# Optimization experiments

Hardware: AMD Instinct MI355X
Metric: run time of the kernel (lower is better)

Reference implementation:

```python
import jax, jax.numpy as jnp
import numpy as np

H = 16
D_MODEL = 1024
D_K = D_MODEL // H
B, S = 4, 2048


def setup_inputs() -> dict:
    key = jax.random.key(0)
    ks = jax.random.split(key, 8)
    scale = 1.0 / np.sqrt(D_MODEL)
    return {
        "query": jax.random.normal(ks[0], (B, S, D_MODEL), dtype=jnp.float32),
        "key": jax.random.normal(ks[1], (B, S, D_MODEL), dtype=jnp.float32),
        "value": jax.random.normal(ks[2], (B, S, D_MODEL), dtype=jnp.float32),
        "A": jnp.zeros((1,), dtype=jnp.float32),
        "Wq": jax.random.normal(ks[3], (D_MODEL, D_MODEL), dtype=jnp.float32) * scale,
        "bq": jnp.zeros((D_MODEL,), dtype=jnp.float32),
        "Wk": jax.random.normal(ks[4], (D_MODEL, D_MODEL), dtype=jnp.float32) * scale,
        "bk": jnp.zeros((D_MODEL,), dtype=jnp.float32),
        "Wv": jax.random.normal(ks[5], (D_MODEL, D_MODEL), dtype=jnp.float32) * scale,
        "bv": jnp.zeros((D_MODEL,), dtype=jnp.float32),
        "Wo": jax.random.normal(ks[6], (D_MODEL, D_MODEL), dtype=jnp.float32) * scale,
        "bo": jnp.zeros((D_MODEL,), dtype=jnp.float32),
    }


def reference(query, key, value, A, Wq, bq, Wk, bk, Wv, bv, Wo, bo):
    nb = query.shape[0]

    def proj(x, W, b):
        # torch Linear: x @ W.T + b, then view(B, S, H, D_K) and transpose -> [B, H, S, D_K]
        y = jnp.einsum('bsd,ed->bse', x, W) + b
        return y.reshape(nb, -1, H, D_K).transpose(0, 2, 1, 3)

    q = proj(query, Wq, bq)
    k = proj(key, Wk, bk)
    v = proj(value, Wv, bv)

    # NOTE: original code has NO 1/sqrt(d_k) scaling, no mask, no dropout.
    scores = jnp.einsum('bhqd,bhkd->bhqk', q, k)  # [B,H,S,S]
    p_attn = jax.nn.softmax(scores, axis=-1)
    x = jnp.einsum('bhqk,bhkd->bhqd', p_attn, v)  # [B,H,S,D_K]

    x = x.transpose(0, 2, 1, 3).reshape(nb, -1, H * D_K)  # [B,S,d_model]
    out = jnp.einsum('bsd,ed->bse', x, Wo) + bo
    loss = jnp.asarray(0.0, dtype=out.dtype)
    return (out, loss)
```

## Files before the change

### kernel.cpp

```cpp
#include <hip/hip_runtime.h>

typedef unsigned short u16;
typedef _Float16 half8 __attribute__((ext_vector_type(8)));
typedef _Float16 h2 __attribute__((ext_vector_type(2)));
typedef float f32x4 __attribute__((ext_vector_type(4)));
typedef u16 u16x4 __attribute__((ext_vector_type(4)));
typedef u16 u16x8 __attribute__((ext_vector_type(8)));

#define MFMAH(a, b, c) __builtin_amdgcn_mfma_f32_16x16x32_f16(a, b, c, 0, 0, 0)

constexpr float LOG2E = 1.44269504088896f;
constexpr float THR = 12.0f;

__device__ __forceinline__ u16 f2h(float f) {
  _Float16 h = (_Float16)f;
  return __builtin_bit_cast(u16, h);
}
__device__ __forceinline__ h2 pkrtz(float a, float b) {
  return __builtin_bit_cast(h2, __builtin_amdgcn_cvt_pkrtz(a, b));
}
__device__ __forceinline__ void gload_lds16(const void* g, void* l) {
  __builtin_amdgcn_global_load_lds(
      (const __attribute__((address_space(1))) void*)g,
      (__attribute__((address_space(3))) void*)l,
      16, 0, 0);
}

__device__ __forceinline__ int swz(int row, int q) { return row * 32 + ((q ^ ((row >> 1) & 3)) << 3); }

__device__ __forceinline__ void conv_block(const float* __restrict__ in,
                                           u16* __restrict__ out, int i) {
  const float4 a = reinterpret_cast<const float4*>(in)[2 * i];
  const float4 b = reinterpret_cast<const float4*>(in)[2 * i + 1];
  u16x8 o;
  o[0] = f2h(a.x); o[1] = f2h(a.y); o[2] = f2h(a.z); o[3] = f2h(a.w);
  o[4] = f2h(b.x); o[5] = f2h(b.y); o[6] = f2h(b.z); o[7] = f2h(b.w);
  reinterpret_cast<u16x8*>(out)[i] = o;
}

__global__ __launch_bounds__(256) void conv_w4(const float* __restrict__ w0,
                                               const float* __restrict__ w1,
                                               const float* __restrict__ w2,
                                               const float* __restrict__ w3,
                                               u16* __restrict__ o0, u16* __restrict__ o1,
                                               u16* __restrict__ o2, u16* __restrict__ o3,
                                               int n8) {
  int i = blockIdx.x * 256 + threadIdx.x;
  const int stride = gridDim.x * 256;
  for (; i < 4 * n8; i += stride) {
    const int sel = i / n8, j = i - sel * n8;
    if (sel == 0) conv_block(w0, o0, j);
    else if (sel == 1) conv_block(w1, o1, j);
    else if (sel == 2) conv_block(w2, o2, j);
    else conv_block(w3, o3, j);
  }
}

__global__ __launch_bounds__(256) void proj_gemm(
    const float* __restrict__ Aq, const float* __restrict__ Ak, const float* __restrict__ Avv,
    const u16* __restrict__ Wq, const u16* __restrict__ Wk, const u16* __restrict__ Wv,
    const float* __restrict__ bq, const float* __restrict__ bk, const float* __restrict__ bv,
    u16* __restrict__ Cq, u16* __restrict__ Ck, u16* __restrict__ Cvv) {
  __shared__ u16 As[2][4096];
  __shared__ u16 Bs[2][4096];
  const int tid = threadIdx.x;
  const int lane = tid & 63, l16 = lane & 15, lhi = lane >> 4;
  const int wid = tid >> 6, wm = wid >> 1, wn = wid & 1;
  const int id = blockIdx.x + (blockIdx.y << 3) + (blockIdx.z << 9);
  const int xcd = id & 7;
  const int slot = id >> 3;
  const int by = ((slot & 7) << 3) | xcd;
  const int rest = slot >> 3;
  const int bx = rest & 7;
  const int z = rest >> 3;
  const int bm0 = by * 128, bn0 = bx * 128;

  const float* Af = (z == 0) ? Aq : ((z == 1) ? Ak : Avv);
  const u16* Bw = (z == 0) ? Wq : ((z == 1) ? Wk : Wv);
  const float* bias = (z == 0) ? bq : ((z == 1) ? bk : bv);
  u16* C = (z == 0) ? Cq : ((z == 1) ? Ck : Cvv);
  const float scale = (z == 0) ? LOG2E : 1.0f;

  const int c0 = tid, c1 = tid + 256;
  const u16* Bg0 = Bw + (size_t)(bn0 + (c0 >> 2)) * 1024 + (((c0 & 3) ^ ((c0 >> 3) & 3)) << 3);
  const u16* Bg1 = Bw + (size_t)(bn0 + (c1 >> 2)) * 1024 + (((c1 & 3) ^ ((c1 >> 3) & 3)) << 3);
  const int arow = tid >> 2, aq = tid & 3;
  const float* Ar = Af + (size_t)(bm0 + arow) * 1024 + aq * 8;
  const int awoff = swz(arow, aq);

  f32x4 acc[4][4] = {};
  float4 an[4];

#define LOADA(kt)                                                          \
  do {                                                                     \
    an[0] = *reinterpret_cast<const float4*>(Ar + (kt));                   \
    an[1] = *reinterpret_cast<const float4*>(Ar + (kt) + 4);               \
    an[2] = *reinterpret_cast<const float4*>(Ar + (kt) + 64 * 1024);       \
    an[3] = *reinterpret_cast<const float4*>(Ar + (kt) + 64 * 1024 + 4);   \
  } while (0)
#define STAGEB(buf, kt)                                                    \
  do {                                                                     \
    gload_lds16(Bg0 + (kt), &Bs[buf][c0 * 8]);                             \
    gload_lds16(Bg1 + (kt), &Bs[buf][c1 * 8]);                             \
  } while (0)
#define WRITEA(buf)                                                        \
  do {                                                                     \
    union { u16x8 u; h2 h[4]; } w0_, w1_;                                  \
    w0_.h[0] = pkrtz(an[0].x, an[0].y); w0_.h[1] = pkrtz(an[0].z, an[0].w);\
    w0_.h[2] = pkrtz(an[1].x, an[1].y); w0_.h[3] = pkrtz(an[1].z, an[1].w);\
    w1_.h[0] = pkrtz(an[2].x, an[2].y); w1_.h[1] = pkrtz(an[2].z, an[2].w);\
    w1_.h[2] = pkrtz(an[3].x, an[3].y); w1_.h[3] = pkrtz(an[3].z, an[3].w);\
    u16* dst_ = &As[buf][awoff];                                           \
    *reinterpret_cast<u16x8*>(dst_) = w0_.u;                               \
    *reinterpret_cast<u16x8*>(dst_ + 64 * 32) = w1_.u;                     \
  } while (0)

  LOADA(0);
  STAGEB(0, 0);
  WRITEA(0);
  __syncthreads();

  for (int ki = 0; ki < 32; ++ki) {
    const int cur = ki & 1, nxt = cur ^ 1;
    if (ki < 31) {
      LOADA((ki + 1) * 32);
      STAGEB(nxt, (ki + 1) * 32);
    }
    half8 af[4], bf[4];
#pragma unroll
    for (int f = 0; f < 4; ++f)
      af[f] = *reinterpret_cast<const half8*>(&As[cur][swz(wm * 64 + f * 16 + l16, lhi)]);
#pragma unroll
    for (int f = 0; f < 4; ++f)
      bf[f] = *reinterpret_cast<const half8*>(&Bs[cur][swz(wn * 64 + f * 16 + l16, lhi)]);
#pragma unroll
    for (int i = 0; i < 4; ++i)
#pragma unroll
      for (int j = 0; j < 4; ++j)
        acc[i][j] = MFMAH(af[i], bf[j], acc[i][j]);
    if (ki < 31) WRITEA(nxt);
    __syncthreads();
  }
#undef LOADA
#undef STAGEB
#undef WRITEA

#pragma unroll
  for (int i = 0; i < 4; ++i) {
    const int m0 = bm0 + wm * 64 + i * 16 + lhi * 4;
#pragma unroll
    for (int j = 0; j < 4; ++j) {
      const int n = bn0 + wn * 64 + j * 16 + l16;
      const float bb = bias[n];
      if (z == 2) {
        u16x4 pack;
#pragma unroll
        for (int r = 0; r < 4; ++r) pack[r] = f2h(acc[i][j][r] + bb);
        const int head = (m0 >> 11) * 16 + (n >> 6);
        const int s0 = m0 & 2047;
        const int d = n & 63;
        const int within =
            ((s0 >> 5) & 1) * 2048 + d * 32 + ((s0 >> 2) & 3) * 8 + ((s0 >> 4) & 1) * 4;
        const int sw = within ^ ((d & 7) << 3);
        const size_t idx = (size_t)head * 131072 + (size_t)(s0 >> 6) * 4096 + sw;
        *reinterpret_cast<u16x4*>(&C[idx]) = pack;
      } else {
#pragma unroll
        for (int r = 0; r < 4; ++r) {
          const int m = m0 + r;
          const size_t idx =
              ((size_t)((m >> 11) * 16 + (n >> 6)) * 2048 + (m & 2047)) * 64 + (n & 63);
          C[idx] = f2h((acc[i][j][r] + bb) * scale);
        }
      }
    }
  }
}

__global__ __launch_bounds__(256) void out_gemm(const u16* __restrict__ A,
                                                const u16* __restrict__ Bw,
                                                const float* __restrict__ bias,
                                                float* __restrict__ C) {
  __shared__ u16 As[2][4096];
  __shared__ u16 Bs[2][4096];
  const int tid = threadIdx.x;
  const int lane = tid & 63, l16 = lane & 15, lhi = lane >> 4;
  const int wid = tid >> 6, wm = wid >> 1, wn = wid & 1;
  const int id = blockIdx.x + (blockIdx.y << 3);
  const int xcd = id & 7, slot = id >> 3;
  const int by = ((slot & 7) << 3) | xcd;
  const int bx = slot >> 3;
  const int bm0 = by * 128, bn0 = bx * 128;

  const int c0 = tid, c1 = tid + 256;
  const u16* Ag0 = A + (size_t)(bm0 + (c0 >> 2)) * 1024 + (((c0 & 3) ^ ((c0 >> 3) & 3)) << 3);
  const u16* Ag1 = A + (size_t)(bm0 + (c1 >> 2)) * 1024 + (((c1 & 3) ^ ((c1 >> 3) & 3)) << 3);
  const u16* Bg0 = Bw + (size_t)(bn0 + (c0 >> 2)) * 1024 + (((c0 & 3) ^ ((c0 >> 3) & 3)) << 3);
  const u16* Bg1 = Bw + (size_t)(bn0 + (c1 >> 2)) * 1024 + (((c1 & 3) ^ ((c1 >> 3) & 3)) << 3);

  f32x4 acc[4][4] = {};

#define STAGE16(buf, kt)                                  \
  do {                                                    \
    gload_lds16(Ag0 + (kt), &As[buf][c0 * 8]);            \
    gload_lds16(Ag1 + (kt), &As[buf][c1 * 8]);            \
    gload_lds16(Bg0 + (kt), &Bs[buf][c0 * 8]);            \
    gload_lds16(Bg1 + (kt), &Bs[buf][c1 * 8]);            \
  } while (0)

  STAGE16(0, 0);
  __syncthreads();
  for (int ki = 0; ki < 32; ++ki) {
    const int cur = ki & 1;
    if (ki < 31) STAGE16(cur ^ 1, (ki + 1) * 32);
    half8 af[4], bf[4];
#pragma unroll
    for (int f = 0; f < 4; ++f)
      af[f] = *reinterpret_cast<const half8*>(&As[cur][swz(wm * 64 + f * 16 + l16, lhi)]);
#pragma unroll
    for (int f = 0; f < 4; ++f)
      bf[f] = *reinterpret_cast<const half8*>(&Bs[cur][swz(wn * 64 + f * 16 + l16, lhi)]);
#pragma unroll
    for (int i = 0; i < 4; ++i)
#pragma unroll
      for (int j = 0; j < 4; ++j)
        acc[i][j] = MFMAH(af[i], bf[j], acc[i][j]);
    __syncthreads();
  }
#undef STAGE16

#pragma unroll
  for (int i = 0; i < 4; ++i) {
    const int m0 = bm0 + wm * 64 + i * 16 + lhi * 4;
#pragma unroll
    for (int j = 0; j < 4; ++j) {
      const int n = bn0 + wn * 64 + j * 16 + l16;
      const float bb = bias[n];
#pragma unroll
      for (int r = 0; r < 4; ++r)
        C[(size_t)(m0 + r) * 1024 + n] = acc[i][j][r] + bb;
    }
  }
  if (id == 0 && tid == 0) C[(size_t)8192 * 1024] = 0.0f;
}

__global__ __launch_bounds__(256, 4) void attn_fwd(const u16* __restrict__ Q,
                                                   const u16* __restrict__ Kh,
                                                   const u16* __restrict__ VL,
                                                   u16* __restrict__ X) {
  __shared__ u16 Ks[2][4096];
  __shared__ u16 Vs[2][4096];

  const int tid = threadIdx.x, lane = tid & 63, w = tid >> 6;
  const int l16 = lane & 15, lhi = lane >> 4;
  const int blk = blockIdx.x;
  const int xcd = blk & 7, wi = blk >> 3;
  const int bh = (xcd << 3) | (wi >> 4);
  const int qt = wi & 15;
  const int b = bh >> 4, h = bh & 15;

  const size_t qrow0 = (size_t)bh * 2048 + qt * 128 + w * 32;
  half8 qf[2][2];
#pragma unroll
  for (int fq = 0; fq < 2; ++fq)
#pragma unroll
    for (int ks = 0; ks < 2; ++ks)
      qf[fq][ks] = *reinterpret_cast<const half8*>(
          &Q[(qrow0 + fq * 16 + l16) * 64 + ks * 32 + lhi * 8]);

  f32x4 o[2][4] = {};
  float mrow[2] = {-1e30f, -1e30f};
  float ssum[2] = {0.0f, 0.0f};

  const u16* Kb = Kh + (size_t)bh * 2048 * 64;
  const u16* VLh = VL + (size_t)bh * 64 * 64 * 32;

#define STAGE_KV(bufidx, tt)                                                      \
  do {                                                                            \
    const int kb0_ = (tt) * 64;                                                   \
    _Pragma("unroll")                                                             \
    for (int ii_ = 0; ii_ < 2; ++ii_) {                                           \
      const int c_ = tid + ii_ * 256;                                             \
      const int r_ = c_ >> 3, cb_ = c_ & 7;                                       \
      gload_lds16(Kb + (size_t)(kb0_ + r_) * 64 + ((cb_ ^ (r_ & 7)) << 3),        \
                  &Ks[bufidx][c_ * 8]);                                           \
      gload_lds16(VLh + (size_t)(tt) * 4096 + c_ * 8, &Vs[bufidx][c_ * 8]);       \
    }                                                                             \
  } while (0)

  STAGE_KV(0, 0);
  __syncthreads();

  for (int t = 0; t < 32; ++t) {
    const int cur = t & 1;
    if (t < 31) STAGE_KV(cur ^ 1, t + 1);
    f32x4 sc[2][4] = {};
    __builtin_amdgcn_s_setprio(1);
#pragma unroll
    for (int fk = 0; fk < 4; ++fk) {
      const int row = fk * 16 + l16;
#pragma unroll
      for (int ks = 0; ks < 2; ++ks) {
        const int off = (row * 64 + ks * 32 + lhi * 8) ^ ((row & 7) << 3);
        const half8 kf = *reinterpret_cast<const half8*>(&Ks[cur][off]);
#pragma unroll
        for (int fq = 0; fq < 2; ++fq) sc[fq][fk] = MFMAH(kf, qf[fq][ks], sc[fq][fk]);
      }
    }
    __builtin_amdgcn_s_setprio(0);
    float lm[2];
#pragma unroll
    for (int fq = 0; fq < 2; ++fq) {
      float a0 = fmaxf(fmaxf(sc[fq][0][0], sc[fq][0][1]), sc[fq][0][2]);
      float a1 = fmaxf(fmaxf(sc[fq][0][3], sc[fq][1][0]), sc[fq][1][1]);
      float a2 = fmaxf(fmaxf(sc[fq][1][2], sc[fq][1][3]), sc[fq][2][0]);
      float a3 = fmaxf(fmaxf(sc[fq][2][1], sc[fq][2][2]), sc[fq][2][3]);
      float a4 = fmaxf(fmaxf(sc[fq][3][0], sc[fq][3][1]), sc[fq][3][2]);
      float b0 = fmaxf(fmaxf(a0, a1), a2);
      float b1 = fmaxf(fmaxf(a3, a4), sc[fq][3][3]);
      lm[fq] = fmaxf(b0, b1);
    }
    const int trig = (lm[0] > mrow[0] + THR) || (lm[1] > mrow[1] + THR);
    if (__any(trig)) {
#pragma unroll
      for (int fq = 0; fq < 2; ++fq) {
        float rm = lm[fq];
        rm = fmaxf(rm, __shfl_xor(rm, 16));
        rm = fmaxf(rm, __shfl_xor(rm, 32));
        const float nm = fmaxf(mrow[fq], rm);
        const float scl = __builtin_amdgcn_exp2f(mrow[fq] - nm);
        mrow[fq] = nm;
        ssum[fq] *= scl;
        float sb[4];
#pragma unroll
        for (int r = 0; r < 4; ++r) sb[r] = __shfl(scl, lhi * 4 + r);
#pragma unroll
        for (int fd = 0; fd < 4; ++fd)
#pragma unroll
          for (int r = 0; r < 4; ++r) o[fq][fd][r] *= sb[r];
      }
    }
    half8 pa2[2][2];
#pragma unroll
    for (int fq = 0; fq < 2; ++fq) {
      union { half8 v[2]; h2 hh[8]; } uu;
#pragma unroll
      for (int fk = 0; fk < 4; ++fk) {
        const float p0 = __builtin_amdgcn_exp2f(sc[fq][fk][0] - mrow[fq]);
        const float p1 = __builtin_amdgcn_exp2f(sc[fq][fk][1] - mrow[fq]);
        const float p2 = __builtin_amdgcn_exp2f(sc[fq][fk][2] - mrow[fq]);
        const float p3 = __builtin_amdgcn_exp2f(sc[fq][fk][3] - mrow[fq]);
        ssum[fq] += (p0 + p1) + (p2 + p3);
        uu.hh[fk * 2 + 0] = pkrtz(p0, p1);
        uu.hh[fk * 2 + 1] = pkrtz(p2, p3);
      }
      pa2[fq][0] = uu.v[0];
      pa2[fq][1] = uu.v[1];
    }
    __builtin_amdgcn_s_setprio(1);
#pragma unroll
    for (int fd = 0; fd < 4; ++fd)
#pragma unroll
      for (int ts = 0; ts < 2; ++ts) {
        const int va = (ts * 2048 + (fd * 16 + l16) * 32 + lhi * 8) ^ ((l16 & 7) << 3);
        const half8 vf = *reinterpret_cast<const half8*>(&Vs[cur][va]);
#pragma unroll
        for (int fq = 0; fq < 2; ++fq) o[fq][fd] = MFMAH(pa2[fq][ts], vf, o[fq][fd]);
      }
    __builtin_amdgcn_s_setprio(0);
    __syncthreads();
  }
#undef STAGE_KV

#pragma unroll
  for (int fq = 0; fq < 2; ++fq) {
    float ss = ssum[fq];
    ss += __shfl_xor(ss, 16);
    ss += __shfl_xor(ss, 32);
    float iv[4];
#pragma unroll
    for (int r = 0; r < 4; ++r) iv[r] = 1.0f / __shfl(ss, lhi * 4 + r);
#pragma unroll
    for (int r = 0; r < 4; ++r) {
      const int q = qt * 128 + w * 32 + fq * 16 + lhi * 4 + r;
#pragma unroll
      for (int fd = 0; fd < 4; ++fd) {
        const int col = h * 64 + fd * 16 + l16;
        X[((size_t)b * 2048 + q) * 1024 + col] = f2h(o[fq][fd][r] * iv[r]);
      }
    }
  }
}

extern "C" void kernel_launch(void* const* d_in, const int* in_sizes, int n_in,
                              void* d_out, int out_size, void* d_ws, size_t ws_size,
                              hipStream_t stream) {
  const float* q_f  = (const float*)d_in[0];
  const float* k_f  = (const float*)d_in[1];
  const float* v_f  = (const float*)d_in[2];
  const float* Wq_f = (const float*)d_in[4];
  const float* bq   = (const float*)d_in[5];
  const float* Wk_f = (const float*)d_in[6];
  const float* bk   = (const float*)d_in[7];
  const float* Wv_f = (const float*)d_in[8];
  const float* bv   = (const float*)d_in[9];
  const float* Wo_f = (const float*)d_in[10];
  const float* bo   = (const float*)d_in[11];

  const int SZ = 4 * 2048 * 1024;
  const int SW = 1024 * 1024;

  u16* ws = (u16*)d_ws;
  u16* wqb = ws;
  u16* wkb = wqb + SW;
  u16* wvb = wkb + SW;
  u16* wob = wvb + SW;
  u16* Qb  = wob + SW;
  u16* Kb  = Qb + SZ;
  u16* VLb = Kb + SZ;
  u16* Xb  = VLb + SZ;
  const size_t need_bytes = (size_t)(4 * SZ + 4 * SW) * 2;
  if (ws_size < need_bytes) return;

  conv_w4<<<1024, 256, 0, stream>>>(Wq_f, Wk_f, Wv_f, Wo_f, wqb, wkb, wvb, wob, SW / 8);

  proj_gemm<<<dim3(8, 64, 3), 256, 0, stream>>>(q_f, k_f, v_f, wqb, wkb, wvb,
                                                bq, bk, bv, Qb, Kb, VLb);

  attn_fwd<<<dim3(1024), 256, 0, stream>>>(Qb, Kb, VLb, Xb);

  out_gemm<<<dim3(8, 64), 256, 0, stream>>>(Xb, wob, bo, (float*)d_out);
}
```

Measured before the change: 212.1 us.

## Triple-buffer projection and output GEMM K-loops with explicit vmcnt barriers

Both projection and output GEMMs go from double- to triple-buffered LDS staging, prefetching two K-tiles ahead. The projection kernel alternates two register sets for the fp32 A loads so the next tile's loads can be in flight while the current one is converted and written. Plain __syncthreads is replaced by a barrier macro that waits only until the most recent tile's loads remain outstanding (vmcnt 6 or 4), keeping prefetches in flight across the barrier. LDS use per block rises from 32KB to 48KB, which may reduce occupancy.

Result: slower. 216.6 us (+2.1%).

```diff
diff --git a/kernel.cpp b/kernel.cpp
--- a/kernel.cpp
+++ b/kernel.cpp
@@ -25,6 +25,14 @@
       (__attribute__((address_space(3))) void*)l,
       16, 0, 0);
 }
+
+#define PIPE_BAR(vmlit)                                                   \
+  do {                                                                    \
+    __builtin_amdgcn_sched_barrier(0);                                    \
+    asm volatile("s_waitcnt lgkmcnt(0) vmcnt(" vmlit ")" ::: "memory");   \
+    __builtin_amdgcn_s_barrier();                                         \
+    __builtin_amdgcn_sched_barrier(0);                                    \
+  } while (0)
 
 __device__ __forceinline__ int swz(int row, int q) { return row * 32 + ((q ^ ((row >> 1) & 3)) << 3); }
 
@@ -61,8 +69,8 @@
     const u16* __restrict__ Wq, const u16* __restrict__ Wk, const u16* __restrict__ Wv,
     const float* __restrict__ bq, const float* __restrict__ bk, const float* __restrict__ bv,
     u16* __restrict__ Cq, u16* __restrict__ Ck, u16* __restrict__ Cvv) {
-  __shared__ u16 As[2][4096];
-  __shared__ u16 Bs[2][4096];
+  __shared__ u16 As[3][4096];
+  __shared__ u16 Bs[3][4096];
   const int tid = threadIdx.x;
   const int lane = tid & 63, l16 = lane & 15, lhi = lane >> 4;
   const int wid = tid >> 6, wm = wid >> 1, wn = wid & 1;
@@ -89,61 +97,73 @@
   const int awoff = swz(arow, aq);
 
   f32x4 acc[4][4] = {};
-  float4 an[4];
-
-#define LOADA(kt)                                                          \
+  float4 anA[4], anB[4];
+
+#define LOADA(set, kt)                                                     \
   do {                                                                     \
-    an[0] = *reinterpret_cast<const float4*>(Ar + (kt));                   \
-    an[1] = *reinterpret_cast<const float4*>(Ar + (kt) + 4);               \
-    an[2] = *reinterpret_cast<const float4*>(Ar + (kt) + 64 * 1024);       \
-    an[3] = *reinterpret_cast<const float4*>(Ar + (kt) + 64 * 1024 + 4);   \
-  } while (0)
-#define STAGEB(buf, kt)                                                    \
+    set[0] = *reinterpret_cast<const float4*>(Ar + (kt));                  \
+    set[1] = *reinterpret_cast<const float4*>(Ar + (kt) + 4);              \
+    set[2] = *reinterpret_cast<const float4*>(Ar + (kt) + 64 * 1024);      \
+    set[3] = *reinterpret_cast<const float4*>(Ar + (kt) + 64 * 1024 + 4);  \
+  } while (0)
+#define STAGEB(sl, kt)                                                     \
   do {                                                                     \
-    gload_lds16(Bg0 + (kt), &Bs[buf][c0 * 8]);                             \
-    gload_lds16(Bg1 + (kt), &Bs[buf][c1 * 8]);                             \
-  } while (0)
-#define WRITEA(buf)                                                        \
+    gload_lds16(Bg0 + (kt), &Bs[sl][c0 * 8]);                              \
+    gload_lds16(Bg1 + (kt), &Bs[sl][c1 * 8]);                              \
+  } while (0)
+#define WRITEA(set, sl)                                                    \
   do {                                                                     \
     union { u16x8 u; h2 h[4]; } w0_, w1_;                                  \
-    w0_.h[0] = pkrtz(an[0].x, an[0].y); w0_.h[1] = pkrtz(an[0].z, an[0].w);\
-    w0_.h[2] = pkrtz(an[1].x, an[1].y); w0_.h[3] = pkrtz(an[1].z, an[1].w);\
-    w1_.h[0] = pkrtz(an[2].x, an[2].y); w1_.h[1] = pkrtz(an[2].z, an[2].w);\
-    w1_.h[2] = pkrtz(an[3].x, an[3].y); w1_.h[3] = pkrtz(an[3].z, an[3].w);\
-    u16* dst_ = &As[buf][awoff];                                           \
+    w0_.h[0] = pkrtz(set[0].x, set[0].y); w0_.h[1] = pkrtz(set[0].z, set[0].w); \
+    w0_.h[2] = pkrtz(set[1].x, set[1].y); w0_.h[3] = pkrtz(set[1].z, set[1].w); \
+    w1_.h[0] = pkrtz(set[2].x, set[2].y); w1_.h[1] = pkrtz(set[2].z, set[2].w); \
+    w1_.h[2] = pkrtz(set[3].x, set[3].y); w1_.h[3] = pkrtz(set[3].z, set[3].w); \
+    u16* dst_ = &As[sl][awoff];                                            \
     *reinterpret_cast<u16x8*>(dst_) = w0_.u;                               \
     *reinterpret_cast<u16x8*>(dst_ + 64 * 32) = w1_.u;                     \
   } while (0)
-
-  LOADA(0);
+#define MFMA_TILE(sl)                                                      \
+  do {                                                                     \
+    half8 af[4], bf[4];                                                    \
+    _Pragma("unroll")                                                      \
+    for (int f = 0; f < 4; ++f)                                            \
+      af[f] = *reinterpret_cast<const half8*>(&As[sl][swz(wm * 64 + f * 16 + l16, lhi)]); \
+    _Pragma("unroll")                                                      \
+    for (int f = 0; f < 4; ++f)                                            \
+      bf[f] = *reinterpret_cast<const half8*>(&Bs[sl][swz(wn * 64 + f * 16 + l16, lhi)]); \
+    _Pragma("unroll")                                                      \
+    for (int i = 0; i < 4; ++i)                                            \
+      _Pragma("unroll")                                                    \
+      for (int j = 0; j < 4; ++j)                                          \
+        acc[i][j] = MFMAH(af[i], bf[j], acc[i][j]);                        \
+  } while (0)
+
   STAGEB(0, 0);
-  WRITEA(0);
-  __syncthreads();
-
-  for (int ki = 0; ki < 32; ++ki) {
-    const int cur = ki & 1, nxt = cur ^ 1;
-    if (ki < 31) {
-      LOADA((ki + 1) * 32);
-      STAGEB(nxt, (ki + 1) * 32);
-    }
-    half8 af[4], bf[4];
-#pragma unroll
-    for (int f = 0; f < 4; ++f)
-      af[f] = *reinterpret_cast<const half8*>(&As[cur][swz(wm * 64 + f * 16 + l16, lhi)]);
-#pragma unroll
-    for (int f = 0; f < 4; ++f)
-      bf[f] = *reinterpret_cast<const half8*>(&Bs[cur][swz(wn * 64 + f * 16 + l16, lhi)]);
-#pragma unroll
-    for (int i = 0; i < 4; ++i)
-#pragma unroll
-      for (int j = 0; j < 4; ++j)
-        acc[i][j] = MFMAH(af[i], bf[j], acc[i][j]);
-    if (ki < 31) WRITEA(nxt);
-    __syncthreads();
+  LOADA(anA, 0);
+  STAGEB(1, 32);
+  LOADA(anB, 32);
+  WRITEA(anA, 0);
+  PIPE_BAR("0");
+
+  for (int t = 0; t < 32; t += 2) {
+    {
+      if (t + 2 < 32) { STAGEB((t + 2) % 3, (t + 2) * 32); LOADA(anA, (t + 2) * 32); }
+      MFMA_TILE(t % 3);
+      if (t + 1 < 32) WRITEA(anB, (t + 1) % 3);
+      if (t + 2 < 32) PIPE_BAR("6"); else PIPE_BAR("0");
+    }
+    {
+      const int u = t + 1;
+      if (u + 2 < 32) { STAGEB((u + 2) % 3, (u + 2) * 32); LOADA(anB, (u + 2) * 32); }
+      MFMA_TILE(u % 3);
+      if (u + 1 < 32) WRITEA(anA, (u + 1) % 3);
+      if (u + 2 < 32) PIPE_BAR("6"); else PIPE_BAR("0");
+    }
   }
 #undef LOADA
 #undef STAGEB
 #undef WRITEA
+#undef MFMA_TILE
 
 #pragma unroll
   for (int i = 0; i < 4; ++i) {
@@ -181,8 +201,8 @@
                                                 const u16* __restrict__ Bw,
                                                 const float* __restrict__ bias,
                                                 float* __restrict__ C) {
-  __shared__ u16 As[2][4096];
-  __shared__ u16 Bs[2][4096];
+  __shared__ u16 As[3][4096];
+  __shared__ u16 Bs[3][4096];
   const int tid = threadIdx.x;
   const int lane = tid & 63, l16 = lane & 15, lhi = lane >> 4;
   const int wid = tid >> 6, wm = wid >> 1, wn = wid & 1;
@@ -200,19 +220,20 @@
 
   f32x4 acc[4][4] = {};
 
-#define STAGE16(buf, kt)                                  \
+#define STAGE16(sl, kt)                                   \
   do {                                                    \
-    gload_lds16(Ag0 + (kt), &As[buf][c0 * 8]);            \
-    gload_lds16(Ag1 + (kt), &As[buf][c1 * 8]);            \
-    gload_lds16(Bg0 + (kt), &Bs[buf][c0 * 8]);            \
-    gload_lds16(Bg1 + (kt), &Bs[buf][c1 * 8]);            \
+    gload_lds16(Ag0 + (kt), &As[sl][c0 * 8]);             \
+    gload_lds16(Ag1 + (kt), &As[sl][c1 * 8]);             \
+    gload_lds16(Bg0 + (kt), &Bs[sl][c0 * 8]);             \
+    gload_lds16(Bg1 + (kt), &Bs[sl][c1 * 8]);             \
   } while (0)
 
   STAGE16(0, 0);
-  __syncthreads();
-  for (int ki = 0; ki < 32; ++ki) {
-    const int cur = ki & 1;
-    if (ki < 31) STAGE16(cur ^ 1, (ki + 1) * 32);
+  STAGE16(1, 32);
+  PIPE_BAR("0");
+  for (int t = 0; t < 32; ++t) {
+    const int cur = t % 3;
+    if (t + 2 < 32) STAGE16((t + 2) % 3, (t + 2) * 32);
     half8 af[4], bf[4];
 #pragma unroll
     for (int f = 0; f < 4; ++f)
@@ -225,7 +246,7 @@
 #pragma unroll
       for (int j = 0; j < 4; ++j)
         acc[i][j] = MFMAH(af[i], bf[j], acc[i][j]);
-    __syncthreads();
+    if (t + 2 < 32) PIPE_BAR("4"); else PIPE_BAR("0");
   }
 #undef STAGE16
 
```
